# Kernel tuning notes

Hardware: AMD Instinct MI355X
Metric: run time of the kernel (lower is better)

The kernel has to match this reference:

```python
import jax, jax.numpy as jnp
import numpy as np

GRID = (8192, 8192)   # 2D lattice, *dims
NDIM = 2              # links.shape[0]
P_LINK = 0.45         # subcritical bond probability -> finite clusters, bounded step count


def setup_inputs() -> dict:
    key = jax.random.key(0)
    k1, k2 = jax.random.split(key)
    # links[i] marks an open bond between site x and its +1 neighbour along axis i
    links = jax.random.uniform(k1, (NDIM,) + GRID) < P_LINK
    seed_idx = jax.random.randint(k2, (NDIM,), 0, GRID[0]).astype(jnp.int32)
    return {"links": links, "seed_idx": seed_idx}


def _flood_fill(links, seed_idx):
    """Faithful port of ClusterSelection.from_seed_idx: BFS-style roll+mask
    expansion iterated to fixed point via lax.while_loop."""
    ndim = links.shape[0]
    grid = links.shape[1:]
    selected0 = jnp.zeros(grid, dtype=bool).at[tuple(seed_idx)].set(True)

    def cond(carry):
        _, is_done, _ = carry
        return ~is_done

    def body(carry):
        sel0, _, steps = carry
        sel = sel0
        for i in range(ndim):  # unrolled over the (small, static) ndim
            # sites whose -1-neighbour or self is selected can use bond i
            links_to_try = sel0 | jnp.roll(sel0, -1, i)
            links_sel = links_to_try & links[i]
            # a taken bond marks both of its endpoints
            links_sel = links_sel | jnp.roll(links_sel, 1, i)
            sel = sel | links_sel
        is_done = (sel ^ sel0).sum() == 0
        return sel, is_done, steps + 1

    sel, _, steps = jax.lax.while_loop(
        cond, body, (selected0, jnp.array(False), jnp.array(0, jnp.int32))
    )
    return sel, steps


def reference(links, seed_idx):
    sel, _steps = _flood_fill(links, seed_idx)
    return sel
```

## Files before the change

### kernel.cpp

```cpp
#include <hip/hip_runtime.h>
#include <stdint.h>

#define GW 8192
#define GMASK 8191
#define PLANE 67108864

__global__ void fill_zero_kernel(int4* __restrict__ out, int n4) {
    int i = blockIdx.x * blockDim.x + threadIdx.x;
    if (i < n4) out[i] = make_int4(0, 0, 0, 0);
}

__global__ void detect_fmt_kernel(const unsigned char* __restrict__ links, int* __restrict__ flag) {
    __shared__ int c12, c3;
    if (threadIdx.x == 0) { c12 = 0; c3 = 0; }
    __syncthreads();
    int l12 = 0, l3 = 0;
    for (int i = threadIdx.x; i < 16384; i += blockDim.x) {
        unsigned char b = links[i];
        if (b) {
            int m = i & 3;
            if (m == 1 || m == 2) l12++;
            else if (m == 3) l3++;
        }
    }
    atomicAdd(&c12, l12);
    atomicAdd(&c3, l3);
    __syncthreads();
    if (threadIdx.x == 0) {
        *flag = (c12 > 0) ? 0 : ((c3 > 0) ? 2 : 1);
    }
}

__global__ void __launch_bounds__(1024)
bfs_kernel(const unsigned char* __restrict__ links8,
           const int* __restrict__ seed_idx,
           unsigned int* __restrict__ out,
           int* __restrict__ q, int qcap,
           const int* __restrict__ flag) {
    __shared__ int s_head, s_cur, s_tail, s_mode;
    const int tid = threadIdx.x;

    if (tid == 0) {
        s_mode = *flag;
        int r = seed_idx[0] & GMASK;
        int c = seed_idx[1] & GMASK;
        int s = r * GW + c;
        atomicExch(&out[s], 1u);
        q[0] = s;
        s_head = 0;
        s_tail = 1;
        s_cur  = 1;
    }
    __syncthreads();
    const int mode = s_mode;
    const int32_t* links32 = (const int32_t*)links8;
    const float*   linksf  = (const float*)links8;

    while (true) {
        int head = s_head;
        int tail = s_cur;
        if (head >= tail) break;

        for (int i = head + tid; i < tail; i += (int)blockDim.x) {
            int s = q[i];
            int r = s >> 13;
            int c = s & GMASK;
            int rp = (r + 1) & GMASK, rm = (r - 1) & GMASK;
            int cp = (c + 1) & GMASK, cm = (c - 1) & GMASK;

            int bidx[4], nbr[4];
            bidx[0] = s;                    nbr[0] = rp * GW + c;
            bidx[1] = rm * GW + c;          nbr[1] = rm * GW + c;
            bidx[2] = PLANE + s;            nbr[2] = r * GW + cp;
            bidx[3] = PLANE + r * GW + cm;  nbr[3] = r * GW + cm;

            #pragma unroll
            for (int k = 0; k < 4; k++) {
                bool open;
                if (mode == 0)      open = links8[bidx[k]] != 0;
                else if (mode == 1) open = links32[bidx[k]] != 0;
                else                open = linksf[bidx[k]] != 0.f;
                if (open) {
                    unsigned int old = atomicExch(&out[nbr[k]], 1u);
                    if (old == 0u) {
                        int pos = atomicAdd(&s_tail, 1);
                        if (pos < qcap) q[pos] = nbr[k];
                    }
                }
            }
        }
        __syncthreads();
        if (tid == 0) { s_head = tail; s_cur = s_tail; }
        __syncthreads();
    }
}

extern "C" void kernel_launch(void* const* d_in, const int* in_sizes, int n_in,
                              void* d_out, int out_size, void* d_ws, size_t ws_size,
                              hipStream_t stream) {
    const unsigned char* links = (const unsigned char*)d_in[0];
    const int* seed = (const int*)d_in[1];

    int* flag = (int*)d_ws;
    int* q    = (int*)((char*)d_ws + 256);
    int  qcap = (int)((ws_size - 256) / sizeof(int));

    int n4 = out_size / 4;
    fill_zero_kernel<<<(n4 + 255) / 256, 256, 0, stream>>>((int4*)d_out, n4);
    detect_fmt_kernel<<<1, 256, 0, stream>>>(links, flag);
    bfs_kernel<<<1, 1024, 0, stream>>>(links, seed, (unsigned int*)d_out, q, qcap, flag);
}
```

Baseline: 675.7 us.

## Replace per-site BFS with bit-packed 64x64 tile flood fill and worklist

```diff
diff --git a/kernel.cpp b/kernel.cpp
--- a/kernel.cpp
+++ b/kernel.cpp
@@ -3,96 +3,202 @@
 
 #define GW 8192
 #define GMASK 8191
-#define PLANE 67108864
-
-__global__ void fill_zero_kernel(int4* __restrict__ out, int n4) {
+#define PLANE 67108864ULL
+#define TPD 128
+#define TMASK 127
+#define NTILES 16384
+#define QCAP 8192
+#define WPR 128
+
+typedef unsigned long long u64;
+typedef unsigned int u32;
+
+__global__ void clear_bitmap_kernel(uint4* __restrict__ p, int n) {
     int i = blockIdx.x * blockDim.x + threadIdx.x;
-    if (i < n4) out[i] = make_int4(0, 0, 0, 0);
+    if (i < n) p[i] = make_uint4(0, 0, 0, 0);
 }
 
 __global__ void detect_fmt_kernel(const unsigned char* __restrict__ links, int* __restrict__ flag) {
-    __shared__ int c12, c3;
-    if (threadIdx.x == 0) { c12 = 0; c3 = 0; }
+    __shared__ int c1, c3;
+    if (threadIdx.x == 0) { c1 = 0; c3 = 0; }
     __syncthreads();
-    int l12 = 0, l3 = 0;
+    int l1 = 0, l3 = 0;
     for (int i = threadIdx.x; i < 16384; i += blockDim.x) {
-        unsigned char b = links[i];
-        if (b) {
+        if (links[i]) {
             int m = i & 3;
-            if (m == 1 || m == 2) l12++;
+            if (m == 1) l1++;
             else if (m == 3) l3++;
         }
     }
-    atomicAdd(&c12, l12);
+    atomicAdd(&c1, l1);
     atomicAdd(&c3, l3);
     __syncthreads();
-    if (threadIdx.x == 0) {
-        *flag = (c12 > 0) ? 0 : ((c3 > 0) ? 2 : 1);
-    }
+    if (threadIdx.x == 0) *flag = (c1 > 0) ? 0 : ((c3 > 0) ? 2 : 1);
+}
+
+__device__ __forceinline__ u32 nib4(u32 w) {
+    return (((w & 0x01010101u) * 0x01020408u) >> 24) & 0xFu;
+}
+__device__ __forceinline__ u64 pack_row_b8(const unsigned char* p) {
+    const uint4* q = (const uint4*)p;
+    u64 w = 0;
+#pragma unroll
+    for (int i = 0; i < 4; i++) {
+        uint4 v = q[i];
+        u64 nb = (u64)(nib4(v.x) | (nib4(v.y) << 4) | (nib4(v.z) << 8) | (nib4(v.w) << 12));
+        w |= nb << (16 * i);
+    }
+    return w;
+}
+__device__ __forceinline__ u64 pack_row_b32(const u32* p) {
+    u64 w = 0;
+#pragma unroll
+    for (int k = 0; k < 16; k++) {
+        uint4 v = ((const uint4*)p)[k];
+        u64 nb = (u64)((v.x != 0) | ((v.y != 0) << 1) | ((v.z != 0) << 2) | ((v.w != 0) << 3));
+        w |= nb << (4 * k);
+    }
+    return w;
 }
 
 __global__ void __launch_bounds__(1024)
-bfs_kernel(const unsigned char* __restrict__ links8,
-           const int* __restrict__ seed_idx,
-           unsigned int* __restrict__ out,
-           int* __restrict__ q, int qcap,
-           const int* __restrict__ flag) {
-    __shared__ int s_head, s_cur, s_tail, s_mode;
+bfs_tiles_kernel(const unsigned char* __restrict__ links8,
+                 const int* __restrict__ seed_idx,
+                 u64* __restrict__ bitmap,
+                 const int* __restrict__ flag) {
+    __shared__ unsigned short q[2][QCAP];
+    __shared__ u32 tflags[NTILES / 32];
+    __shared__ int s_cnt, s_ncnt, s_head, s_flip, s_mode;
+
     const int tid = threadIdx.x;
-
+    const int ln  = tid & 63;
+
+    for (int i = tid; i < NTILES / 32; i += 1024) tflags[i] = 0;
     if (tid == 0) {
         s_mode = *flag;
-        int r = seed_idx[0] & GMASK;
-        int c = seed_idx[1] & GMASK;
-        int s = r * GW + c;
-        atomicExch(&out[s], 1u);
-        q[0] = s;
-        s_head = 0;
-        s_tail = 1;
-        s_cur  = 1;
+        int sr = seed_idx[0] & GMASK, sc = seed_idx[1] & GMASK;
+        atomicOr(&bitmap[(u64)sr * WPR + (sc >> 6)], 1ull << (sc & 63));
+        int t = (sr >> 6) * TPD + (sc >> 6);
+        tflags[t >> 5] = 1u << (t & 31);
+        q[0][0] = (unsigned short)t;
+        s_cnt = 1; s_ncnt = 0; s_head = 0; s_flip = 0;
     }
     __syncthreads();
+
     const int mode = s_mode;
-    const int32_t* links32 = (const int32_t*)links8;
-    const float*   linksf  = (const float*)links8;
-
+    const unsigned char* p0b = links8;
+    const unsigned char* p1b = links8 + PLANE;
+    const u32* p0w = (const u32*)links8;
+    const u32* p1w = (const u32*)(links8 + PLANE * 4);
+
+    int safety = 0;
     while (true) {
-        int head = s_head;
-        int tail = s_cur;
-        if (head >= tail) break;
-
-        for (int i = head + tid; i < tail; i += (int)blockDim.x) {
-            int s = q[i];
-            int r = s >> 13;
-            int c = s & GMASK;
-            int rp = (r + 1) & GMASK, rm = (r - 1) & GMASK;
-            int cp = (c + 1) & GMASK, cm = (c - 1) & GMASK;
-
-            int bidx[4], nbr[4];
-            bidx[0] = s;                    nbr[0] = rp * GW + c;
-            bidx[1] = rm * GW + c;          nbr[1] = rm * GW + c;
-            bidx[2] = PLANE + s;            nbr[2] = r * GW + cp;
-            bidx[3] = PLANE + r * GW + cm;  nbr[3] = r * GW + cm;
-
-            #pragma unroll
-            for (int k = 0; k < 4; k++) {
-                bool open;
-                if (mode == 0)      open = links8[bidx[k]] != 0;
-                else if (mode == 1) open = links32[bidx[k]] != 0;
-                else                open = linksf[bidx[k]] != 0.f;
-                if (open) {
-                    unsigned int old = atomicExch(&out[nbr[k]], 1u);
-                    if (old == 0u) {
-                        int pos = atomicAdd(&s_tail, 1);
-                        if (pos < qcap) q[pos] = nbr[k];
-                    }
+        const int flip = s_flip;
+        const int cnt  = s_cnt;
+
+        auto enq = [&](int t) {
+            u32 bit = 1u << (t & 31);
+            u32 old = atomicOr(&tflags[t >> 5], bit);
+            if (!(old & bit)) {
+                int p = atomicAdd(&s_ncnt, 1);
+                if (p < QCAP) q[flip ^ 1][p] = (unsigned short)t;
+            }
+        };
+
+        while (true) {
+            int pos = 0;
+            if (ln == 0) pos = atomicAdd(&s_head, 1);
+            pos = __shfl(pos, 0);
+            if (pos >= cnt) break;
+            int t = q[flip][pos];
+            int tR = t >> 7, tC = t & TMASK;
+            if (ln == 0) atomicAnd(&tflags[t >> 5], ~(1u << (t & 31)));
+            __threadfence_block();
+
+            const int gr = tR * 64 + ln;
+            u64* wp = &bitmap[(u64)gr * WPR + tC];
+            u64 loaded = *(volatile u64*)wp;
+
+            u64 l0, l1;
+            if (mode == 0) {
+                l0 = pack_row_b8(p0b + (u64)gr * GW + tC * 64);
+                l1 = pack_row_b8(p1b + (u64)gr * GW + tC * 64);
+            } else {
+                l0 = pack_row_b32(p0w + (u64)gr * GW + tC * 64);
+                l1 = pack_row_b32(p1w + (u64)gr * GW + tC * 64);
+            }
+
+            u64 sel = loaded;
+            while (true) {
+                u64 old = sel;
+                sel |= (sel & l1) << 1;
+                sel |= (sel >> 1) & l1;
+                u64 sb = sel & l0;
+                u64 up = __shfl_up(sb, 1);
+                if (ln > 0) sel |= up;
+                u64 dn = __shfl_down(sel, 1);
+                if (ln < 63) sel |= dn & l0;
+                if (__ballot(sel != old) == 0ull) break;
+            }
+
+            u64 newbits = sel & ~loaded;
+            if (newbits) atomicOr(wp, newbits);
+
+            const int c0 = tC * 64;
+            bool rnew = false, lnew = false;
+            if ((sel >> 63) & (l1 >> 63) & 1ull) {
+                u64 old = atomicOr(&bitmap[(u64)gr * WPR + ((tC + 1) & TMASK)], 1ull);
+                rnew = !(old & 1ull);
+            }
+            {
+                u64 lcol = (u64)((c0 - 1) & GMASK);
+                bool lopen = (mode == 0) ? (p1b[(u64)gr * GW + lcol] != 0)
+                                         : (p1w[(u64)gr * GW + lcol] != 0);
+                if ((sel & 1ull) && lopen) {
+                    u64 old = atomicOr(&bitmap[(u64)gr * WPR + ((tC - 1) & TMASK)], 1ull << 63);
+                    lnew = !(old & (1ull << 63));
                 }
             }
+            u64 rmask = __ballot(rnew), lmask = __ballot(lnew);
+
+            const int ga = (tR * 64 - 1) & GMASK;
+            bool bopen = (mode == 0) ? (p0b[(u64)ga * GW + c0 + ln] != 0)
+                                     : (p0w[(u64)ga * GW + c0 + ln] != 0);
+            u64 top_sel = __shfl(sel, 0);
+            u64 umask = __ballot(bopen && ((top_sel >> ln) & 1));
+            u64 unew = 0;
+            if (ln == 0 && umask) {
+                u64 old = atomicOr(&bitmap[(u64)ga * WPR + tC], umask);
+                unew = umask & ~old;
+            }
+            u64 dmask = sel & l0;
+            const int gb = (tR * 64 + 64) & GMASK;
+            u64 dnew = 0;
+            if (ln == 63 && dmask) {
+                u64 old = atomicOr(&bitmap[(u64)gb * WPR + tC], dmask);
+                dnew = dmask & ~old;
+            }
+
+            if (ln == 0  && rmask) enq(tR * TPD + ((tC + 1) & TMASK));
+            if (ln == 1  && lmask) enq(tR * TPD + ((tC - 1) & TMASK));
+            if (ln == 0  && unew)  enq(((tR - 1) & TMASK) * TPD + tC);
+            if (ln == 63 && dnew)  enq(((tR + 1) & TMASK) * TPD + tC);
         }
+
         __syncthreads();
-        if (tid == 0) { s_head = tail; s_cur = s_tail; }
+        if (tid == 0) { s_cnt = s_ncnt; s_ncnt = 0; s_head = 0; s_flip ^= 1; }
         __syncthreads();
-    }
+        if (s_cnt == 0) break;
+        if (++safety > 30000) break;
+    }
+}
+
+__global__ void writeout_kernel(const u64* __restrict__ bitmap, int4* __restrict__ out) {
+    int g = blockIdx.x * blockDim.x + threadIdx.x;
+    int site0 = g << 2;
+    u64 w = bitmap[site0 >> 6];
+    u32 b = (u32)(w >> (site0 & 63)) & 0xFu;
+    out[g] = make_int4(b & 1, (b >> 1) & 1, (b >> 2) & 1, (b >> 3) & 1);
 }
 
 extern "C" void kernel_launch(void* const* d_in, const int* in_sizes, int n_in,
@@ -101,12 +207,11 @@
     const unsigned char* links = (const unsigned char*)d_in[0];
     const int* seed = (const int*)d_in[1];
 
-    int* flag = (int*)d_ws;
-    int* q    = (int*)((char*)d_ws + 256);
-    int  qcap = (int)((ws_size - 256) / sizeof(int));
-
-    int n4 = out_size / 4;
-    fill_zero_kernel<<<(n4 + 255) / 256, 256, 0, stream>>>((int4*)d_out, n4);
+    int* flag   = (int*)d_ws;
+    u64* bitmap = (u64*)((char*)d_ws + 4096);
+
+    clear_bitmap_kernel<<<2048, 256, 0, stream>>>((uint4*)bitmap, 524288);
     detect_fmt_kernel<<<1, 256, 0, stream>>>(links, flag);
-    bfs_kernel<<<1, 1024, 0, stream>>>(links, seed, (unsigned int*)d_out, q, qcap, flag);
-}
+    bfs_tiles_kernel<<<1, 1024, 0, stream>>>(links, seed, bitmap, flag);
+    writeout_kernel<<<65536, 256, 0, stream>>>(bitmap, (int4*)d_out);
+}
```

Measured after the change: 683.0 us. About the same (+1.1%).
